# Kernel tuning notes

Hardware: AMD Instinct MI355X
Metric: run time of the kernel (lower is better)

## Reference

```python
import jax, jax.numpy as jnp
import numpy as np

B, N = 2, 256
RC = 6.0
BOX = 12.0
# (center_radius, eta) for G2; kappas for G3; (eta, zeta, lambda) for G4/G5
G2_PARAMS = [(rs, eta) for rs in (0.0, 2.0) for eta in (0.1, 1.0)]
G3_KAPPAS = [1.0, 2.0]
G45_PARAMS = [(eta, zeta, lam) for eta in (0.01, 0.1) for zeta in (1.0, 4.0) for lam in (-1.0, 1.0)]


def _fc(r, rc):
    # Behler cosine cutoff: 0.5*(cos(pi r / rc) + 1) for r < rc, else 0
    return 0.5 * (jnp.cos(jnp.pi * r / rc) + 1.0) * (r < rc)


def setup_inputs() -> dict:
    key = jax.random.key(0)
    k1, k2 = jax.random.split(key)
    atomic_numbers = jax.random.randint(k1, (N,), 1, 10).astype(jnp.float32)
    coordinates = jax.random.uniform(k2, (B, N, 3), dtype=jnp.float32) * BOX
    return {"atomic_numbers": atomic_numbers, "coordinates": coordinates}


def reference(atomic_numbers, coordinates):
    b, n, _ = coordinates.shape
    # r_ij vector = x_i - x_j, matching coords.unsqueeze(-2) - coords.unsqueeze(-3)
    dvec = coordinates[:, :, None, :] - coordinates[:, None, :, :]        # [B,N,N,3]
    sq = jnp.sum(dvec * dvec, axis=-1)                                    # [B,N,N]
    pair_mask = ~jnp.eye(n, dtype=bool)                                   # j != i
    sq_safe = jnp.where(pair_mask, sq, 1.0)
    r = jnp.where(pair_mask, jnp.sqrt(sq_safe), 0.0)                      # [B,N,N]
    fcr = _fc(r, RC) * pair_mask                                          # cutoff, self excluded

    feats = [jnp.broadcast_to(atomic_numbers, (b, n))]
    # G1: sum_j fc(r_ij)
    feats.append(jnp.sum(fcr, axis=-1))
    # G2: sum_j exp(-eta*(r_ij - Rs)^2) * fc(r_ij)
    for rs, eta in G2_PARAMS:
        feats.append(jnp.sum(jnp.exp(-eta * (r - rs) ** 2) * fcr, axis=-1))
    # G3: sum_j cos(kappa * r_ij) * fc(r_ij)
    for kappa in G3_KAPPAS:
        feats.append(jnp.sum(jnp.cos(kappa * r) * fcr, axis=-1))

    # shared angular (triplet) quantities, each [B,N,N,N]
    dot = jnp.einsum('bijc,bikc->bijk', dvec, dvec)
    denom = r[:, :, :, None] * r[:, :, None, :]
    cos_t = dot / jnp.where(denom > 0, denom, 1.0)
    sq_ij = sq[:, :, :, None]
    sq_ik = sq[:, :, None, :]
    sq_jk = sq[:, None, :, :]
    sq3 = sq_ij + sq_ik + sq_jk
    sq2 = sq_ij + sq_ik
    # fc products: fcr already zero on the diagonal, so fc3 vanishes whenever
    # j==i, k==i, or j==k (full triplet mask for G4)
    fc3 = fcr[:, :, :, None] * fcr[:, :, None, :] * fcr[:, None, :, :]
    fc2 = fcr[:, :, :, None] * fcr[:, :, None, :] * pair_mask[None, None, :, :]

    # G4: 2^(1-zeta) sum_{j!=k} (1+lam*cos)^zeta exp(-eta*(rij^2+rik^2+rjk^2)) fc fc fc
    for eta, zeta, lam in G45_PARAMS:
        ang = jnp.maximum(1.0 + lam * cos_t, 0.0) ** zeta
        feats.append((2.0 ** (1.0 - zeta)) * jnp.sum(ang * jnp.exp(-eta * sq3) * fc3, axis=(-2, -1)))
    # G5: 2^(1-zeta) sum_{j!=k} (1+lam*cos)^zeta exp(-eta*(rij^2+rik^2)) fc fc
    for eta, zeta, lam in G45_PARAMS:
        ang = jnp.maximum(1.0 + lam * cos_t, 0.0) ** zeta
        feats.append((2.0 ** (1.0 - zeta)) * jnp.sum(ang * jnp.exp(-eta * sq2) * fc2, axis=(-2, -1)))

    return jnp.stack(feats, axis=-1)  # [B, N, 24]
```

## Files before the change

### kernel.cpp

```cpp
#include <hip/hip_runtime.h>
#include <math.h>

#define NN 256
#define NF 24
#define RCUT 6.0f
#define PI_F 3.14159265358979323846f
#define CS 0.27415568f

__device__ __forceinline__ float fc_poly(float u) {
    float p = 1.0438378e-9f;
    p = fmaf(p, u, -1.3778659e-7f);
    p = fmaf(p, u,  1.2400794e-5f);
    p = fmaf(p, u, -6.9444444e-4f);
    p = fmaf(p, u,  2.0833333e-2f);
    p = fmaf(p, u, -0.25f);
    p = fmaf(p, u,  1.0f);
    return p;
}

__global__ __launch_bounds__(512, 4) void feat_kernel(
    const float* __restrict__ Z,
    const float* __restrict__ coords,
    float* __restrict__ out)
{
    const int i = blockIdx.x, b = blockIdx.y, e = blockIdx.z;
    const int tid = threadIdx.x, lane = tid & 63, wave = tid >> 6;
    const float ETA = e ? 0.1f : 0.01f;

    __shared__ float4 geo[NN + 128];
    __shared__ float2 ab[NN + 128];
    __shared__ int   wave_cnt[4];
    __shared__ float rad[4][7];
    __shared__ float red[8][8][4];
    __shared__ float mom[64][36];
    __shared__ float momsum[36];

    const float* cb = coords + (size_t)b * NN * 3;
    const float xi = cb[i * 3 + 0], yi = cb[i * 3 + 1], zi = cb[i * 3 + 2];

    float dx = 0, dy = 0, dz = 0, r2 = 0, r = 0, fc = 0;
    bool incut = false;
    if (tid < NN) {
        const float xj = cb[tid * 3 + 0], yj = cb[tid * 3 + 1], zj = cb[tid * 3 + 2];
        dx = xi - xj; dy = yi - yj; dz = zi - zj;
        r2 = dx * dx + dy * dy + dz * dz;
        r  = sqrtf(r2);
        incut = (tid != i) && (r < RCUT);
        fc = incut ? 0.5f * (__cosf((PI_F / RCUT) * r) + 1.0f) : 0.0f;
        if (e == 0) {
            float racc[7];
            racc[0] = fc;
            racc[1] = __expf(-0.1f * r2) * fc;
            racc[2] = __expf(-1.0f * r2) * fc;
            const float d = r - 2.0f;
            racc[3] = __expf(-0.1f * d * d) * fc;
            racc[4] = __expf(-1.0f * d * d) * fc;
            racc[5] = __cosf(r) * fc;
            racc[6] = __cosf(2.0f * r) * fc;
#pragma unroll
            for (int t = 0; t < 7; t++) {
                float v = racc[t];
                for (int off = 32; off > 0; off >>= 1) v += __shfl_down(v, off, 64);
                if (lane == 0) rad[wave][t] = v;
            }
        }
        const unsigned long long bal = __ballot(incut);
        if (lane == 0) wave_cnt[wave] = __popcll(bal);
    }
    __syncthreads();

    const int m = wave_cnt[0] + wave_cnt[1] + wave_cnt[2] + wave_cnt[3];
    if (tid < NN && incut) {
        const unsigned long long bal = __ballot(incut);
        int base = 0;
#pragma unroll
        for (int w = 0; w < 4; w++) if (w < wave) base += wave_cnt[w];
        const int p = base + __popcll(bal & ((1ULL << lane) - 1ULL));
        const float rinv = 1.0f / r;
        geo[p] = make_float4(dx * rinv, dy * rinv, dz * rinv, r);
        ab[p]  = make_float2(fc * __expf(-ETA * r2), r2);
    }
    __syncthreads();
    const int Rext = (m >= 2) ? ((m - 1) >> 1) : 0;
    for (int s = tid; s < Rext; s += 512) { geo[m + s] = geo[s]; ab[m + s] = ab[s]; }
    __syncthreads();

    float acc[4] = {0.0f, 0.0f, 0.0f, 0.0f};
    if (m >= 2) {
        const int Rfull = (m - 1) >> 1;
        const int tlo = 1 + ((Rfull * wave) >> 3);
        const int thi = (Rfull * (wave + 1)) >> 3;
        const int mh = m >> 1;
        const bool doHalf = (wave == 7) && ((m & 1) == 0);
        for (int rnd = 0; rnd < 4; ++rnd) {
            const int jj = lane + (rnd << 6);
            if (jj >= m) break;
            const float4 gj = geo[jj];
            const float2 aj = ab[jj];
            const float r2j = aj.y;
            const float gw2 = -2.0f * gj.w;
            const int tend = thi + ((doHalf && jj < mh) ? 1 : 0);
            for (int t = tlo; t <= tend; ++t) {
                const int kk = jj + ((t > thi) ? mh : t);
                const float4 g = geo[kk];
                const float2 a = ab[kk];
                const float cost = fmaf(gj.x, g.x, fmaf(gj.y, g.y, gj.z * g.z));
                const float s = fmaf(gw2 * g.w, cost, r2j + a.y);
                const float pfc = fc_poly(CS * s);
                const float fcjk = (s < 36.0f) ? pfc : 0.0f;
                const float w3 = (aj.x * a.x) * (fcjk * __expf(-ETA * s));
                const float c1m = 1.0f - cost, c1p = 1.0f + cost;
                const float c2m = c1m * c1m, c2p = c1p * c1p;
                acc[0] += c1m * w3;          acc[1] += c1p * w3;
                acc[2] += c2m * c2m * w3;    acc[3] += c2p * c2p * w3;
            }
        }
    }
#pragma unroll
    for (int t = 0; t < 4; t++) {
        float v = acc[t];
        v += __shfl_down(v, 32, 64);
        v += __shfl_down(v, 16, 64);
        v += __shfl_down(v, 8, 64);
        acc[t] = v;
    }
    if (lane < 8) {
#pragma unroll
        for (int t = 0; t < 4; t++) red[wave][lane][t] = acc[t];
    }

    if (wave == 0) {
        float mm[36];
#pragma unroll
        for (int q = 0; q < 36; q++) mm[q] = 0.0f;
        for (int rnd = 0; rnd < 4; ++rnd) {
            const int jj = lane + (rnd << 6);
            if (jj >= m) break;
            const float4 g = geo[jj];
            const float w = ab[jj].x;
            const float x = g.x, y = g.y, z = g.z;
            mm[0] += w;
            const float wx = w * x, wy = w * y, wz = w * z;
            mm[1] += wx; mm[2] += wy; mm[3] += wz;
            const float wxx = wx * x, wxy = wx * y, wxz = wx * z;
            const float wyy = wy * y, wyz = wy * z, wzz = wz * z;
            mm[4] += wxx; mm[5] += wxy; mm[6] += wxz;
            mm[7] += wyy; mm[8] += wyz; mm[9] += wzz;
            const float wxxx = wxx * x, wxxy = wxx * y, wxxz = wxx * z;
            const float wxyy = wxy * y, wxyz = wxy * z, wxzz = wxz * z;
            const float wyyy = wyy * y, wyyz = wyy * z, wyzz = wyz * z, wzzz = wzz * z;
            mm[10] += wxxx; mm[11] += wxxy; mm[12] += wxxz; mm[13] += wxyy;
            mm[14] += wxyz; mm[15] += wxzz; mm[16] += wyyy; mm[17] += wyyz;
            mm[18] += wyzz; mm[19] += wzzz;
            mm[20] += wxxx * x; mm[21] += wxxx * y; mm[22] += wxxx * z;
            mm[23] += wxxy * y; mm[24] += wxxy * z; mm[25] += wxxz * z;
            mm[26] += wxyy * y; mm[27] += wxyy * z; mm[28] += wxyz * z;
            mm[29] += wxzz * z; mm[30] += wyyy * y; mm[31] += wyyy * z;
            mm[32] += wyyz * z; mm[33] += wyzz * z; mm[34] += wzzz * z;
            mm[35] = fmaf(w, w, mm[35]);
        }
#pragma unroll
        for (int q = 0; q < 36; q++) mom[lane][q] = mm[q];
        if (lane < 36) {
            float v0 = 0, v1 = 0, v2 = 0, v3 = 0;
#pragma unroll
            for (int j = 0; j < 64; j += 4) {
                v0 += mom[j + 0][lane]; v1 += mom[j + 1][lane];
                v2 += mom[j + 2][lane]; v3 += mom[j + 3][lane];
            }
            momsum[lane] = (v0 + v1) + (v2 + v3);
        }
    }
    __syncthreads();

    float* ob = out + ((size_t)b * NN + i) * NF;
    if (tid < 32) {
        const int f = tid >> 3, s = tid & 7;
        float v = 0.0f;
#pragma unroll
        for (int w = 0; w < 8; w++) v += red[w][s][f];
        v += __shfl_down(v, 4, 8);
        v += __shfl_down(v, 2, 8);
        v += __shfl_down(v, 1, 8);
        if (s == 0) {
            v *= (f >= 2) ? 0.25f : 2.0f;
            ob[8 + 4 * e + f] = v;
        }
    } else if (tid < 36) {
        const int sub = tid - 32;
        const float* M = momsum;
        const float S0 = M[0] * M[0];
        const float S1 = M[1] * M[1] + M[2] * M[2] + M[3] * M[3];
        const float S2 = M[4] * M[4] + M[7] * M[7] + M[9] * M[9]
                       + 2.f * (M[5] * M[5] + M[6] * M[6] + M[8] * M[8]);
        const float S3 = M[10] * M[10] + M[16] * M[16] + M[19] * M[19]
                       + 3.f * (M[11] * M[11] + M[12] * M[12] + M[13] * M[13]
                              + M[15] * M[15] + M[17] * M[17] + M[18] * M[18])
                       + 6.f * M[14] * M[14];
        const float S4 = M[20] * M[20] + M[30] * M[30] + M[34] * M[34]
                       + 4.f * (M[21] * M[21] + M[22] * M[22] + M[26] * M[26]
                              + M[29] * M[29] + M[31] * M[31] + M[33] * M[33])
                       + 6.f * (M[23] * M[23] + M[25] * M[25] + M[32] * M[32])
                       + 12.f * (M[24] * M[24] + M[27] * M[27] + M[28] * M[28]);
        const float D = M[35];
        const float lam = (sub & 1) ? 1.0f : -1.0f;
        float v;
        if (sub < 2) v = S0 + lam * S1 - (1.0f + lam) * D;
        else         v = 0.125f * (S0 + 6.f * S2 + S4 + lam * 4.f * (S1 + S3)
                                   - ((sub == 3) ? 16.f * D : 0.0f));
        ob[16 + 4 * e + sub] = v;
    } else if (e == 0 && tid >= 36 && tid < 43) {
        const int t = tid - 36;
        ob[1 + t] = rad[0][t] + rad[1][t] + rad[2][t] + rad[3][t];
    } else if (e == 0 && tid == 43) {
        ob[0] = Z[i];
    }
}

extern "C" void kernel_launch(void* const* d_in, const int* in_sizes, int n_in,
                              void* d_out, int out_size, void* d_ws, size_t ws_size,
                              hipStream_t stream) {
    const float* Z = (const float*)d_in[0];
    const float* coords = (const float*)d_in[1];
    float* out = (float*)d_out;
    feat_kernel<<<dim3(NN, 2, 2), dim3(512), 0, stream>>>(Z, coords, out);
}
```

Baseline: 63.31 us.

## Fuse both eta variants into one block to share triplet geometry work

Removes the grid z-dimension over eta, so each block computes the G4 and G5 features for both eta values at once. The triplet loop now shares the cosine, the jk distance and the cutoff polynomial, and evaluates two exponentials into eight accumulators. The moment accumulation is split across two waves, one per eta. This halves the block count and avoids recomputing shared geometry, at the cost of more registers per thread and fewer blocks available to fill the GPU.

```diff
diff --git a/kernel.cpp b/kernel.cpp
--- a/kernel.cpp
+++ b/kernel.cpp
@@ -23,17 +23,16 @@
     const float* __restrict__ coords,
     float* __restrict__ out)
 {
-    const int i = blockIdx.x, b = blockIdx.y, e = blockIdx.z;
+    const int i = blockIdx.x, b = blockIdx.y;
     const int tid = threadIdx.x, lane = tid & 63, wave = tid >> 6;
-    const float ETA = e ? 0.1f : 0.01f;
 
     __shared__ float4 geo[NN + 128];
-    __shared__ float2 ab[NN + 128];
+    __shared__ float4 ab2[NN + 128];
     __shared__ int   wave_cnt[4];
     __shared__ float rad[4][7];
-    __shared__ float red[8][8][4];
-    __shared__ float mom[64][36];
-    __shared__ float momsum[36];
+    __shared__ float red[8][8][8];
+    __shared__ float mom[2][64][36];
+    __shared__ float momsum[2][36];
 
     const float* cb = coords + (size_t)b * NN * 3;
     const float xi = cb[i * 3 + 0], yi = cb[i * 3 + 1], zi = cb[i * 3 + 2];
@@ -47,7 +46,7 @@
         r  = sqrtf(r2);
         incut = (tid != i) && (r < RCUT);
         fc = incut ? 0.5f * (__cosf((PI_F / RCUT) * r) + 1.0f) : 0.0f;
-        if (e == 0) {
+        {
             float racc[7];
             racc[0] = fc;
             racc[1] = __expf(-0.1f * r2) * fc;
@@ -78,14 +77,14 @@
         const int p = base + __popcll(bal & ((1ULL << lane) - 1ULL));
         const float rinv = 1.0f / r;
         geo[p] = make_float4(dx * rinv, dy * rinv, dz * rinv, r);
-        ab[p]  = make_float2(fc * __expf(-ETA * r2), r2);
+        ab2[p] = make_float4(fc * __expf(-0.01f * r2), fc * __expf(-0.1f * r2), r2, 0.0f);
     }
     __syncthreads();
     const int Rext = (m >= 2) ? ((m - 1) >> 1) : 0;
-    for (int s = tid; s < Rext; s += 512) { geo[m + s] = geo[s]; ab[m + s] = ab[s]; }
-    __syncthreads();
-
-    float acc[4] = {0.0f, 0.0f, 0.0f, 0.0f};
+    for (int sx = tid; sx < Rext; sx += 512) { geo[m + sx] = geo[sx]; ab2[m + sx] = ab2[sx]; }
+    __syncthreads();
+
+    float acc[8] = {0, 0, 0, 0, 0, 0, 0, 0};
     if (m >= 2) {
         const int Rfull = (m - 1) >> 1;
         const int tlo = 1 + ((Rfull * wave) >> 3);
@@ -96,28 +95,35 @@
             const int jj = lane + (rnd << 6);
             if (jj >= m) break;
             const float4 gj = geo[jj];
-            const float2 aj = ab[jj];
-            const float r2j = aj.y;
+            const float4 aj = ab2[jj];
+            const float r2j = aj.z;
+            const float W0j = aj.x, W1j = aj.y;
             const float gw2 = -2.0f * gj.w;
             const int tend = thi + ((doHalf && jj < mh) ? 1 : 0);
             for (int t = tlo; t <= tend; ++t) {
                 const int kk = jj + ((t > thi) ? mh : t);
                 const float4 g = geo[kk];
-                const float2 a = ab[kk];
+                const float4 a = ab2[kk];
                 const float cost = fmaf(gj.x, g.x, fmaf(gj.y, g.y, gj.z * g.z));
-                const float s = fmaf(gw2 * g.w, cost, r2j + a.y);
+                const float s = fmaf(gw2 * g.w, cost, r2j + a.z);
                 const float pfc = fc_poly(CS * s);
                 const float fcjk = (s < 36.0f) ? pfc : 0.0f;
-                const float w3 = (aj.x * a.x) * (fcjk * __expf(-ETA * s));
+                const float t0 = fcjk * __expf(-0.01f * s);
+                const float t1 = fcjk * __expf(-0.1f * s);
+                const float w30 = (W0j * a.x) * t0;
+                const float w31 = (W1j * a.y) * t1;
                 const float c1m = 1.0f - cost, c1p = 1.0f + cost;
                 const float c2m = c1m * c1m, c2p = c1p * c1p;
-                acc[0] += c1m * w3;          acc[1] += c1p * w3;
-                acc[2] += c2m * c2m * w3;    acc[3] += c2p * c2p * w3;
+                const float c4m = c2m * c2m, c4p = c2p * c2p;
+                acc[0] += c1m * w30;  acc[1] += c1p * w30;
+                acc[2] += c4m * w30;  acc[3] += c4p * w30;
+                acc[4] += c1m * w31;  acc[5] += c1p * w31;
+                acc[6] += c4m * w31;  acc[7] += c4p * w31;
             }
         }
     }
 #pragma unroll
-    for (int t = 0; t < 4; t++) {
+    for (int t = 0; t < 8; t++) {
         float v = acc[t];
         v += __shfl_down(v, 32, 64);
         v += __shfl_down(v, 16, 64);
@@ -126,10 +132,10 @@
     }
     if (lane < 8) {
 #pragma unroll
-        for (int t = 0; t < 4; t++) red[wave][lane][t] = acc[t];
-    }
-
-    if (wave == 0) {
+        for (int t = 0; t < 8; t++) red[wave][lane][t] = acc[t];
+    }
+
+    if (wave < 2) {
         float mm[36];
 #pragma unroll
         for (int q = 0; q < 36; q++) mm[q] = 0.0f;
@@ -137,7 +143,8 @@
             const int jj = lane + (rnd << 6);
             if (jj >= m) break;
             const float4 g = geo[jj];
-            const float w = ab[jj].x;
+            const float4 a = ab2[jj];
+            const float w = wave ? a.y : a.x;
             const float x = g.x, y = g.y, z = g.z;
             mm[0] += w;
             const float wx = w * x, wy = w * y, wz = w * z;
@@ -160,21 +167,21 @@
             mm[35] = fmaf(w, w, mm[35]);
         }
 #pragma unroll
-        for (int q = 0; q < 36; q++) mom[lane][q] = mm[q];
+        for (int q = 0; q < 36; q++) mom[wave][lane][q] = mm[q];
         if (lane < 36) {
             float v0 = 0, v1 = 0, v2 = 0, v3 = 0;
 #pragma unroll
             for (int j = 0; j < 64; j += 4) {
-                v0 += mom[j + 0][lane]; v1 += mom[j + 1][lane];
-                v2 += mom[j + 2][lane]; v3 += mom[j + 3][lane];
+                v0 += mom[wave][j + 0][lane]; v1 += mom[wave][j + 1][lane];
+                v2 += mom[wave][j + 2][lane]; v3 += mom[wave][j + 3][lane];
             }
-            momsum[lane] = (v0 + v1) + (v2 + v3);
+            momsum[wave][lane] = (v0 + v1) + (v2 + v3);
         }
     }
     __syncthreads();
 
     float* ob = out + ((size_t)b * NN + i) * NF;
-    if (tid < 32) {
+    if (tid < 64) {
         const int f = tid >> 3, s = tid & 7;
         float v = 0.0f;
 #pragma unroll
@@ -183,12 +190,14 @@
         v += __shfl_down(v, 2, 8);
         v += __shfl_down(v, 1, 8);
         if (s == 0) {
-            v *= (f >= 2) ? 0.25f : 2.0f;
-            ob[8 + 4 * e + f] = v;
-        }
-    } else if (tid < 36) {
-        const int sub = tid - 32;
-        const float* M = momsum;
+            const int e = f >> 2, ff = f & 3;
+            v *= (ff >= 2) ? 0.25f : 2.0f;
+            ob[8 + 4 * e + ff] = v;
+        }
+    } else if (tid < 72) {
+        const int sub = tid - 64;
+        const int e = sub >> 2, ss = sub & 3;
+        const float* M = momsum[e];
         const float S0 = M[0] * M[0];
         const float S1 = M[1] * M[1] + M[2] * M[2] + M[3] * M[3];
         const float S2 = M[4] * M[4] + M[7] * M[7] + M[9] * M[9]
@@ -203,16 +212,16 @@
                        + 6.f * (M[23] * M[23] + M[25] * M[25] + M[32] * M[32])
                        + 12.f * (M[24] * M[24] + M[27] * M[27] + M[28] * M[28]);
         const float D = M[35];
-        const float lam = (sub & 1) ? 1.0f : -1.0f;
+        const float lam = (ss & 1) ? 1.0f : -1.0f;
         float v;
-        if (sub < 2) v = S0 + lam * S1 - (1.0f + lam) * D;
-        else         v = 0.125f * (S0 + 6.f * S2 + S4 + lam * 4.f * (S1 + S3)
-                                   - ((sub == 3) ? 16.f * D : 0.0f));
-        ob[16 + 4 * e + sub] = v;
-    } else if (e == 0 && tid >= 36 && tid < 43) {
-        const int t = tid - 36;
+        if (ss < 2) v = S0 + lam * S1 - (1.0f + lam) * D;
+        else        v = 0.125f * (S0 + 6.f * S2 + S4 + lam * 4.f * (S1 + S3)
+                                  - ((ss == 3) ? 16.f * D : 0.0f));
+        ob[16 + 4 * e + ss] = v;
+    } else if (tid < 79) {
+        const int t = tid - 72;
         ob[1 + t] = rad[0][t] + rad[1][t] + rad[2][t] + rad[3][t];
-    } else if (e == 0 && tid == 43) {
+    } else if (tid == 79) {
         ob[0] = Z[i];
     }
 }
@@ -223,5 +232,5 @@
     const float* Z = (const float*)d_in[0];
     const float* coords = (const float*)d_in[1];
     float* out = (float*)d_out;
-    feat_kernel<<<dim3(NN, 2, 2), dim3(512), 0, stream>>>(Z, coords, out);
+    feat_kernel<<<dim3(NN, 2), dim3(512), 0, stream>>>(Z, coords, out);
 }
```

Result: no change. 62.64 us (-1.1%).
